# Optimization experiments

Measured on AMD Instinct MI355X. Metric: run time of the kernel, lower is better.

Reference implementation:

```python
import jax, jax.numpy as jnp
import numpy as np

LEN = 128
HIDDEN = 64
B, N = 256, 2048
LN_EPS = 1e-3  # keras LayerNormalization default epsilon
NEG_FILL = -1.0e9


def setup_inputs() -> dict:
    key = jax.random.key(0)
    k_in, k_m, k_w1, k_w2 = jax.random.split(key, 4)
    inputs = jax.random.normal(k_in, (B, N, LEN), dtype=jnp.float32)
    mask = jax.random.randint(k_m, (B, N), 0, 2) > 0
    # He-normal init for Dense kernels, zeros for biases (keras defaults)
    W1 = jax.random.normal(k_w1, (LEN, HIDDEN), dtype=jnp.float32) * np.sqrt(2.0 / LEN)
    b1 = jnp.zeros((HIDDEN,), dtype=jnp.float32)
    W2 = jax.random.normal(k_w2, (HIDDEN, LEN), dtype=jnp.float32) * np.sqrt(2.0 / HIDDEN)
    b2 = jnp.zeros((LEN,), dtype=jnp.float32)
    gamma = jnp.ones((LEN,), dtype=jnp.float32)
    beta = jnp.zeros((LEN,), dtype=jnp.float32)
    return {"inputs": inputs, "mask": mask, "W1": W1, "b1": b1,
            "W2": W2, "b2": b2, "gamma": gamma, "beta": beta}


def reference(inputs, mask, W1, b1, W2, b2, gamma, beta):
    # MLP: Dense -> Dense -> LayerNorm -> ReLU (weights shared over nodes)
    h = jnp.einsum('bnd,dh->bnh', inputs, W1) + b1          # [B,N,HIDDEN]
    h = jnp.einsum('bnh,hd->bnd', h, W2) + b2               # [B,N,LEN]
    mu = jnp.mean(h, axis=-1, keepdims=True)
    var = jnp.mean(jnp.square(h - mu), axis=-1, keepdims=True)
    h = (h - mu) * jax.lax.rsqrt(var + LN_EPS) * gamma + beta
    x = jax.nn.relu(h)                                      # [B,N,LEN]
    # masked fill (masked-out nodes set to large negative before max-pool)
    x = jnp.where(mask[:, :, None], x, NEG_FILL)
    # global max-pool over all N nodes, broadcast back, concat local+global
    x_pool = jnp.max(x, axis=1, keepdims=True)              # [B,1,LEN]
    x_tile = jnp.broadcast_to(x_pool, x.shape)              # [B,N,LEN]
    return jnp.concatenate([x, x_tile], axis=-1)            # [B,N,2*LEN]
```

## Files before the change

### kernel.cpp

```cpp
#include <hip/hip_runtime.h>
#include <hip/hip_bf16.h>

#define NEG_FILL -1.0e9f

using bf16x8 = __attribute__((ext_vector_type(8))) short;
using f32x4  = __attribute__((ext_vector_type(4))) float;

static __device__ __forceinline__ short f2bf(float f) {
    union { float f; unsigned u; } a; a.f = f;
    unsigned r = a.u + 0x7FFFu + ((a.u >> 16) & 1u);
    return (short)(r >> 16);
}

static __device__ __forceinline__ bf16x8 pack8(float4 a, float4 b) {
    union { __hip_bfloat162 h[4]; bf16x8 v; } u;
    u.h[0] = __float22bfloat162_rn({a.x, a.y});
    u.h[1] = __float22bfloat162_rn({a.z, a.w});
    u.h[2] = __float22bfloat162_rn({b.x, b.y});
    u.h[3] = __float22bfloat162_rn({b.z, b.w});
    return u.v;
}


__global__ __launch_bounds__(256) void k_prep(
    const float* __restrict__ W1, const float* __restrict__ b1,
    const float* __restrict__ W2, const float* __restrict__ b2,
    short* __restrict__ WT, float* __restrict__ beff, int* __restrict__ pool)
{
    int blk = blockIdx.x, tid = threadIdx.x;
    if (blk < 128) {
        pool[blk * 256 + tid] = __float_as_int(NEG_FILL);
        return;
    }
    if (blk < 192) {
        int e = (blk - 128) * 256 + tid;
        int n = e >> 7, k = e & 127;
        float s = 0.f;
        #pragma unroll 8
        for (int h = 0; h < 64; ++h) s = fmaf(W1[k * 64 + h], W2[h * 128 + n], s);
        WT[e] = f2bf(s);
    } else if (tid < 128) {
        float s = b2[tid];
        for (int h = 0; h < 64; ++h) s = fmaf(b1[h], W2[h * 128 + tid], s);
        beff[tid] = s;
    }
}

__global__ __launch_bounds__(256) void k_main(
    const float* __restrict__ X, const int* __restrict__ mask,
    const short* __restrict__ WT, const float* __restrict__ beff,
    const float* __restrict__ gamma, const float* __restrict__ beta,
    float* __restrict__ out, int* __restrict__ pool)
{
    __shared__ short Ws[128][136];
    __shared__ int pool_s[128];

    const int tid = threadIdx.x;
    const int rowbase = blockIdx.x * 64;

    if (tid < 128) pool_s[tid] = __float_as_int(NEG_FILL);

    #pragma unroll
    for (int i = 0; i < 8; ++i) {
        int g = tid + i * 256;
        int n = g >> 4, koff = (g & 15) * 8;
        *(bf16x8*)&Ws[n][koff] = *(const bf16x8*)(WT + g * 8);
    }

    const int wave = tid >> 6, lane = tid & 63;
    const int c = lane & 15, q = lane >> 4;
    const int rowloc = wave * 16 + c;
    const float* __restrict__ xrow = X + (size_t)(rowbase + rowloc) * 128;

    float be[8], ga[8], bt[8];
    #pragma unroll
    for (int t = 0; t < 8; ++t) {
        int n = t * 16 + c;
        be[t] = beff[n]; ga[t] = gamma[n]; bt[t] = beta[n];
    }

    __syncthreads();

    f32x4 acc[8];
    const f32x4 zero = {0.f, 0.f, 0.f, 0.f};
    #pragma unroll
    for (int t = 0; t < 8; ++t) acc[t] = zero;

    #pragma unroll
    for (int kk = 0; kk < 4; ++kk) {
        float4 x0 = *(const float4*)(xrow + kk * 32 + q * 8);
        float4 x1 = *(const float4*)(xrow + kk * 32 + q * 8 + 4);
        bf16x8 a = pack8(x0, x1);
        #pragma unroll
        for (int t = 0; t < 8; ++t) {
            bf16x8 b = *(const bf16x8*)&Ws[t * 16 + c][kk * 32 + q * 8];
            acc[t] = __builtin_amdgcn_mfma_f32_16x16x32_bf16(a, b, acc[t], 0, 0, 0);
        }
    }

    float v[8][4];
    #pragma unroll
    for (int t = 0; t < 8; ++t)
        #pragma unroll
        for (int r = 0; r < 4; ++r) v[t][r] = acc[t][r] + be[t];

    #pragma unroll
    for (int r = 0; r < 4; ++r) {
        float s = 0.f, s2 = 0.f;
        #pragma unroll
        for (int t = 0; t < 8; ++t) { s += v[t][r]; s2 = fmaf(v[t][r], v[t][r], s2); }
        #pragma unroll
        for (int m = 1; m < 16; m <<= 1) {
            s  += __shfl_xor(s,  m, 64);
            s2 += __shfl_xor(s2, m, 64);
        }
        float mu  = s * (1.f / 128.f);
        float var = s2 * (1.f / 128.f) - mu * mu;
        float rs  = rsqrtf(var + 1e-3f);
        int rg = rowbase + wave * 16 + q * 4 + r;
        int mk = mask[rg];
        #pragma unroll
        for (int t = 0; t < 8; ++t) {
            float y = fmaf((v[t][r] - mu) * rs, ga[t], bt[t]);
            y = fmaxf(y, 0.f);
            y = mk ? y : NEG_FILL;
            v[t][r] = y;
            out[(size_t)rg * 256 + t * 16 + c] = y;
        }
    }

    #pragma unroll
    for (int t = 0; t < 8; ++t) {
        float pm = fmaxf(fmaxf(v[t][0], v[t][1]), fmaxf(v[t][2], v[t][3]));
        pm = fmaxf(pm, __shfl_xor(pm, 16, 64));
        pm = fmaxf(pm, __shfl_xor(pm, 32, 64));
        if (q == 0) atomicMax(&pool_s[t * 16 + c], __float_as_int(pm));
    }
    __syncthreads();
    if (tid < 128) {
        int b = rowbase >> 11;
        atomicMax(&pool[b * 128 + tid], pool_s[tid]);
    }
}

__global__ __launch_bounds__(256) void k_bcast(
    const f32x4* __restrict__ pool4, f32x4* __restrict__ out4)
{
    unsigned base = blockIdx.x * 256 + threadIdx.x;
    #pragma unroll
    for (int i = 0; i < 16; ++i) {
        unsigned idx = base + (unsigned)i * (4096u * 256u);
        unsigned row = idx >> 5;
        unsigned c4  = idx & 31;
        unsigned b   = row >> 11;
        f32x4 pv = pool4[b * 32 + c4];
        __builtin_nontemporal_store(pv, &out4[(size_t)row * 64 + 32 + c4]);
    }
}

extern "C" void kernel_launch(void* const* d_in, const int* in_sizes, int n_in,
                              void* d_out, int out_size, void* d_ws, size_t ws_size,
                              hipStream_t stream)
{
    const float* X     = (const float*)d_in[0];
    const int*   mask  = (const int*)d_in[1];
    const float* W1    = (const float*)d_in[2];
    const float* b1    = (const float*)d_in[3];
    const float* W2    = (const float*)d_in[4];
    const float* b2    = (const float*)d_in[5];
    const float* gamma = (const float*)d_in[6];
    const float* beta  = (const float*)d_in[7];
    float* out = (float*)d_out;

    short* WT   = (short*)d_ws;
    float* beff = (float*)((char*)d_ws + 32768);
    int*   pool = (int*)((char*)d_ws + 33280);

    k_prep<<<193, 256, 0, stream>>>(W1, b1, W2, b2, WT, beff, pool);
    k_main<<<8192, 256, 0, stream>>>(X, mask, WT, beff, gamma, beta, out, pool);
    k_bcast<<<4096, 256, 0, stream>>>((const f32x4*)pool, (f32x4*)out);
}
```

Measured before the change: 723.6 us.

## Fuse pool broadcast into main kernel via last-block-per-batch counter

Removes the separate broadcast kernel. Each main-kernel block increments a per-batch counter after merging its pool maxima, and the last of the 32 blocks for a batch reads the final pool and writes the broadcast half of the output for all 2048 rows of that batch. This saves a launch and lets the broadcast writes overlap the compute of other blocks. In exchange, a single block must write a whole batch's broadcast region, which can leave a serialized tail at the end of the grid.

```diff
diff --git a/kernel.cpp b/kernel.cpp
--- a/kernel.cpp
+++ b/kernel.cpp
@@ -25,11 +25,13 @@
 __global__ __launch_bounds__(256) void k_prep(
     const float* __restrict__ W1, const float* __restrict__ b1,
     const float* __restrict__ W2, const float* __restrict__ b2,
-    short* __restrict__ WT, float* __restrict__ beff, int* __restrict__ pool)
+    short* __restrict__ WT, float* __restrict__ beff, int* __restrict__ pool,
+    int* __restrict__ cnt)
 {
     int blk = blockIdx.x, tid = threadIdx.x;
     if (blk < 128) {
         pool[blk * 256 + tid] = __float_as_int(NEG_FILL);
+        if (blk == 0) cnt[tid] = 0;
         return;
     }
     if (blk < 192) {
@@ -50,13 +52,15 @@
     const float* __restrict__ X, const int* __restrict__ mask,
     const short* __restrict__ WT, const float* __restrict__ beff,
     const float* __restrict__ gamma, const float* __restrict__ beta,
-    float* __restrict__ out, int* __restrict__ pool)
+    float* __restrict__ out, int* __restrict__ pool, int* __restrict__ cnt)
 {
     __shared__ short Ws[128][136];
-    __shared__ int pool_s[128];
+    __shared__ __align__(16) int pool_s[128];
+    __shared__ int lastflag;
 
     const int tid = threadIdx.x;
     const int rowbase = blockIdx.x * 64;
+    const int bidx = rowbase >> 11;
 
     if (tid < 128) pool_s[tid] = __float_as_int(NEG_FILL);
 
@@ -137,24 +141,25 @@
         if (q == 0) atomicMax(&pool_s[t * 16 + c], __float_as_int(pm));
     }
     __syncthreads();
-    if (tid < 128) {
-        int b = rowbase >> 11;
-        atomicMax(&pool[b * 128 + tid], pool_s[tid]);
-    }
-}
+    if (tid < 128) atomicMax(&pool[bidx * 128 + tid], pool_s[tid]);
 
-__global__ __launch_bounds__(256) void k_bcast(
-    const f32x4* __restrict__ pool4, f32x4* __restrict__ out4)
-{
-    unsigned base = blockIdx.x * 256 + threadIdx.x;
-    #pragma unroll
-    for (int i = 0; i < 16; ++i) {
-        unsigned idx = base + (unsigned)i * (4096u * 256u);
-        unsigned row = idx >> 5;
-        unsigned c4  = idx & 31;
-        unsigned b   = row >> 11;
-        f32x4 pv = pool4[b * 32 + c4];
-        __builtin_nontemporal_store(pv, &out4[(size_t)row * 64 + 32 + c4]);
+    __threadfence();
+    __syncthreads();
+    if (tid == 0) lastflag = (atomicAdd(&cnt[bidx], 1) == 31);
+    __syncthreads();
+    if (!lastflag) return;
+
+    if (tid < 128)
+        pool_s[tid] = atomicMax(&pool[bidx * 128 + tid], __float_as_int(NEG_FILL));
+    __syncthreads();
+
+    const f32x4 pv = ((const f32x4*)pool_s)[tid & 31];
+    f32x4* __restrict__ out4 = (f32x4*)out;
+    const size_t rb = (size_t)bidx * 2048;
+    #pragma unroll 8
+    for (int it = 0; it < 256; ++it) {
+        size_t row = rb + (size_t)it * 8 + (tid >> 5);
+        __builtin_nontemporal_store(pv, &out4[row * 64 + 32 + (tid & 31)]);
     }
 }
 
@@ -175,8 +180,8 @@
     short* WT   = (short*)d_ws;
     float* beff = (float*)((char*)d_ws + 32768);
     int*   pool = (int*)((char*)d_ws + 33280);
+    int*   cnt  = (int*)((char*)d_ws + 164352);
 
-    k_prep<<<193, 256, 0, stream>>>(W1, b1, W2, b2, WT, beff, pool);
-    k_main<<<8192, 256, 0, stream>>>(X, mask, WT, beff, gamma, beta, out, pool);
-    k_bcast<<<4096, 256, 0, stream>>>((const f32x4*)pool, (f32x4*)out);
+    k_prep<<<193, 256, 0, stream>>>(W1, b1, W2, b2, WT, beff, pool, cnt);
+    k_main<<<8192, 256, 0, stream>>>(X, mask, WT, beff, gamma, beta, out, pool, cnt);
 }
```

New measurement: 2.184 ms. 202% more time.
